# Performance work log

Measured on AMD Instinct MI355X. Metric: run time of the kernel, lower is better.

The kernel has to match this reference:

```python
import jax, jax.numpy as jnp
import numpy as np

D = 256        # d_model
DL = 256       # d_latent
S = 2048       # seq_len
B = 8          # batches
F = 8192       # facts per batch (padded)
MAXPOS = 4096
MAXPRED = 1024
NROLE = 64 + 2 # role_emb rows


def setup_inputs() -> dict:
    key = jax.random.key(0)
    ks = jax.random.split(key, 16)
    def nrm(k, shape, s=0.02):
        return jax.random.normal(k, shape, jnp.float32) * s
    return {
        "pos_emb": nrm(ks[0], (MAXPOS, D)),
        "pred_emb": nrm(ks[1], (MAXPRED, D)),
        "role_emb": nrm(ks[2], (NROLE, D)),
        "w1": nrm(ks[3], (3 * D, 2 * D)), "b1": jnp.zeros((2 * D,), jnp.float32),
        "w2": nrm(ks[4], (2 * D, D)),     "b2": jnp.zeros((D,), jnp.float32),
        "ln_g": jnp.ones((D,), jnp.float32), "ln_b": jnp.zeros((D,), jnp.float32),
        "lw1": nrm(ks[5], (D, DL)), "lb1": jnp.zeros((DL,), jnp.float32),
        "lw2": nrm(ks[6], (DL, DL)), "lb2": jnp.zeros((DL,), jnp.float32),
        "pred_idx": jax.random.randint(ks[7], (B, F), 0, MAXPRED),
        "a0": jax.random.randint(ks[8], (B, F), 0, S),
        "a1": jax.random.randint(ks[9], (B, F), 0, S),
        "role_idx": jax.random.randint(ks[10], (B, F), 0, NROLE),
        "is_role": jax.random.randint(ks[11], (B, F), 0, 2).astype(jnp.int32),
        "add_rev": jax.random.randint(ks[12], (B, F), 0, 2).astype(jnp.int32),
        "mask": jax.random.randint(ks[13], (B, F), 0, 2).astype(jnp.int32),
        "seq_len": S,
    }


def reference(pos_emb, pred_emb, role_emb, w1, b1, w2, b2, ln_g, ln_b,
              lw1, lb1, lw2, lb2,
              pred_idx, a0, a1, role_idx, is_role, add_rev, mask, seq_len):
    nodes = pos_emb[:seq_len]                 # [S, D] shared across batches
    pe = pred_emb[pred_idx]                   # [B, F, D]
    n0 = nodes[a0]                            # [B, F, D]
    n1 = nodes[a1]                            # [B, F, D]
    re = role_emb[role_idx]                   # [B, F, D]

    role_b = is_role.astype(bool)
    valid = mask.astype(bool)

    third = jnp.where(role_b[..., None], re, n1)
    x_fwd = jnp.concatenate([n0, pe, third], axis=-1)   # [B, F, 3D]
    x_rev = jnp.concatenate([n1, pe, n0], axis=-1)      # [B, F, 3D]

    def mlp(x):
        h = jax.nn.gelu(x @ w1 + b1, approximate=False)
        return h @ w2 + b2

    msg_fwd = mlp(x_fwd)                      # [B, F, D]
    msg_rev = mlp(x_rev)                      # [B, F, D]

    w_fwd = valid[..., None].astype(msg_fwd.dtype)
    w_rev = (valid & (~role_b) & add_rev.astype(bool))[..., None].astype(msg_rev.dtype)
    tgt_fwd = jnp.where(role_b, a0, a1)       # role msgs go to tok=a0, binary to a1

    def scat(msg, idx, w):
        return jax.ops.segment_sum(msg * w, idx, num_segments=seq_len)

    agg = jax.vmap(scat)(msg_fwd, tgt_fwd, w_fwd)
    agg = agg + jax.vmap(scat)(msg_rev, a0, w_rev)      # [B, S, D]

    x = nodes[None, :, :] + agg
    mu = jnp.mean(x, axis=-1, keepdims=True)
    var = jnp.mean(jnp.square(x - mu), axis=-1, keepdims=True)
    x = (x - mu) / jnp.sqrt(var + 1e-5) * ln_g + ln_b   # LayerNorm

    pooled = jnp.mean(x, axis=1)              # [B, D]
    h = jax.nn.gelu(pooled @ lw1 + lb1, approximate=False)
    return h @ lw2 + lb2                      # [B, DL]
```

## Files before the change

kernel.cpp:

```cpp
#include <hip/hip_runtime.h>
#include <hip/hip_bf16.h>
#include <cstdint>

#define S_LEN 2048
#define DIM   256
#define NBAT  8
#define NEDGE 65536
#define HID   512
#define INDIM 768

#define OFF_AGG   0u
#define OFF_POOL  16777216u
#define OFF_CNT   16785408u
#define OFF_NODES 16785664u
#define OFF_PRED  17834240u
#define OFF_ROLE  18358528u
#define OFF_W1P   18392576u
#define OFF_W2P   19179008u
#define OFF_FWD   19441152u
#define OFF_REV   19703296u
#define ZERO_BYTES 16785664u

typedef short bshort8 __attribute__((ext_vector_type(8)));
typedef float floatx4 __attribute__((ext_vector_type(4)));
typedef ushort ushort4v __attribute__((ext_vector_type(4)));

__device__ __forceinline__ float gelu_f(float x) {
  return 0.5f * x * (1.0f + erff(x * 0.70710678118654752f));
}
__device__ __forceinline__ ushort f2bf(float v) {
  __hip_bfloat16 h = __float2bfloat16(v);
  return *reinterpret_cast<ushort*>(&h);
}

#define Z4 1049104
#define T4 200832
#define WN 524288
__global__ void prep_all(const float* __restrict__ pos, const float* __restrict__ pred,
                         const float* __restrict__ role,
                         const float* __restrict__ w1, const float* __restrict__ w2,
                         unsigned char* __restrict__ ws) {
  int i = blockIdx.x * blockDim.x + threadIdx.x;
  if (i < Z4) {
    reinterpret_cast<float4*>(ws)[i] = float4{0.f, 0.f, 0.f, 0.f};
    return;
  }
  i -= Z4;
  if (i < T4) {
    const int NN4 = 131072, NP4 = 65536;
    float4 v;
    if (i < NN4) v = reinterpret_cast<const float4*>(pos)[i];
    else if (i < NN4 + NP4) v = reinterpret_cast<const float4*>(pred)[i - NN4];
    else v = reinterpret_cast<const float4*>(role)[i - NN4 - NP4];
    ushort4v h;
    h.x = f2bf(v.x); h.y = f2bf(v.y); h.z = f2bf(v.z); h.w = f2bf(v.w);
    *reinterpret_cast<ushort4v*>((ushort*)(ws + OFF_NODES) + (i << 2)) = h;
    return;
  }
  i -= T4;
  if (i < WN) {
    ushort* W1p = (ushort*)(ws + OFF_W1P);
    ushort* W2p = (ushort*)(ws + OFF_W2P);
    const int N1 = INDIM * HID;
    if (i < N1) {
      int k = i >> 9, n = i & 511;
      W1p[(((k >> 3) << 9) + n) * 8 + (k & 7)] = f2bf(w1[i]);
    } else {
      int j = i - N1;
      int k = j >> 8, n = j & 255;
      W2p[(((k >> 3) << 8) + n) * 8 + (k & 7)] = f2bf(w2[j]);
    }
  }
}

__global__ void build_lists(const int* __restrict__ mask, const int* __restrict__ is_role,
                            const int* __restrict__ add_rev,
                            int* __restrict__ fwd, int* __restrict__ rev, int* __restrict__ cnt) {
  int e = blockIdx.x * blockDim.x + threadIdx.x;
  int lane = threadIdx.x & 63;
  bool c0 = mask[e] != 0;
  bool c1 = c0 && !is_role[e] && add_rev[e];
  unsigned long long b0 = __ballot(c0);
  unsigned long long b1m = __ballot(c1);
  unsigned long long lt = (1ull << lane) - 1ull;
  int base0 = 0, base1 = 0;
  if (lane == 0) {
    base0 = atomicAdd(&cnt[0], __popcll(b0));
    base1 = atomicAdd(&cnt[1], __popcll(b1m));
  }
  base0 = __shfl(base0, 0);
  base1 = __shfl(base1, 0);
  if (c0) fwd[base0 + __popcll(b0 & lt)] = e;
  if (c1) rev[base1 + __popcll(b1m & lt)] = e;
}

#define HSTR_E 520
__global__ __launch_bounds__(512, 4)
void mlp_kernel(const int* __restrict__ cnt, const int* __restrict__ fwd, const int* __restrict__ rev,
                const int* __restrict__ a0, const int* __restrict__ a1,
                const int* __restrict__ pred_idx, const int* __restrict__ role_idx,
                const int* __restrict__ is_role,
                const ushort* __restrict__ T,
                const ushort* __restrict__ W1p, const ushort* __restrict__ W2p,
                const float* __restrict__ b1, const float* __restrict__ b2,
                float* __restrict__ agg) {
  __shared__ ushort Hs[64 * HSTR_E];
  __shared__ int ltgt[64];
  __shared__ int lbat[64];
  __shared__ uint loff[64][3];

  const int tid = threadIdx.x;
  const int nf = cnt[0], nr = cnt[1];
  const int total = nf + nr;
  const int row0 = blockIdx.x * 64;
  if (row0 >= total) return;

  if (tid < 64) {
    int grow = row0 + tid;
    int tgt = -1, bb = 0; uint o0 = 0, o1 = 0, o2 = 0;
    if (grow < total) {
      bool rv = grow >= nf;
      int e = rv ? rev[grow - nf] : fwd[grow];
      bb = e >> 13;
      int A0 = a0[e], A1 = a1[e];
      o1 = 524288u + ((uint)pred_idx[e] << 8);
      if (rv)              { o0 = (uint)A1 << 8; o2 = (uint)A0 << 8;                      tgt = A0; }
      else if (is_role[e]) { o0 = (uint)A0 << 8; o2 = 786432u + ((uint)role_idx[e] << 8); tgt = A0; }
      else                 { o0 = (uint)A0 << 8; o2 = (uint)A1 << 8;                      tgt = A1; }
    }
    ltgt[tid] = tgt; lbat[tid] = bb;
    loff[tid][0] = o0; loff[tid][1] = o1; loff[tid][2] = o2;
  }
  __syncthreads();

  const int lane = tid & 63, wave = tid >> 6;
  const int wm = wave >> 2, wn = wave & 3;
  const int l15 = lane & 15, kb = lane >> 4;
  const int m0 = wm * 32 + l15;
  const int m1 = m0 + 16;

  const uint o00 = loff[m0][0], o01 = loff[m0][1], o02 = loff[m0][2];
  const uint o10 = loff[m1][0], o11 = loff[m1][1], o12 = loff[m1][2];

  floatx4 acc1[2][8];
#pragma unroll
  for (int fm = 0; fm < 2; ++fm)
#pragma unroll
    for (int fn = 0; fn < 8; ++fn) acc1[fm][fn] = (floatx4){0.f, 0.f, 0.f, 0.f};

  const int kcb = kb * 8;
  bshort8 xb0 = *reinterpret_cast<const bshort8*>(T + o00 + kcb);
  bshort8 xb1 = *reinterpret_cast<const bshort8*>(T + o10 + kcb);
#pragma unroll 1
  for (int k0 = 0; k0 < INDIM; k0 += 32) {
    int k1 = k0 + 32;
    uint po0 = (k1 < 256) ? o00 : (k1 < 512) ? o01 : o02;
    uint po1 = (k1 < 256) ? o10 : (k1 < 512) ? o11 : o12;
    int kc1 = (k1 & 255) + kcb;
    bshort8 nx0 = *reinterpret_cast<const bshort8*>(T + po0 + kc1);
    bshort8 nx1 = *reinterpret_cast<const bshort8*>(T + po1 + kc1);

    const ushort* wp = W1p + ((((k0 >> 3) + kb) << 9) + wn * 128 + l15) * 8;
#pragma unroll
    for (int fn = 0; fn < 8; ++fn) {
      bshort8 wv = *reinterpret_cast<const bshort8*>(wp + (fn << 7));
      acc1[0][fn] = __builtin_amdgcn_mfma_f32_16x16x32_bf16(wv, xb0, acc1[0][fn], 0, 0, 0);
      acc1[1][fn] = __builtin_amdgcn_mfma_f32_16x16x32_bf16(wv, xb1, acc1[1][fn], 0, 0, 0);
    }
    xb0 = nx0; xb1 = nx1;
  }

#pragma unroll
  for (int fm = 0; fm < 2; ++fm) {
    int m = fm ? m1 : m0;
#pragma unroll
    for (int fn = 0; fn < 8; ++fn) {
      int n0 = wn * 128 + fn * 16 + kb * 4;
      float4 bb4 = *reinterpret_cast<const float4*>(b1 + n0);
      ushort4v hv;
      hv.x = f2bf(gelu_f(acc1[fm][fn][0] + bb4.x));
      hv.y = f2bf(gelu_f(acc1[fm][fn][1] + bb4.y));
      hv.z = f2bf(gelu_f(acc1[fm][fn][2] + bb4.z));
      hv.w = f2bf(gelu_f(acc1[fm][fn][3] + bb4.w));
      *reinterpret_cast<ushort4v*>(Hs + m * HSTR_E + n0) = hv;
    }
  }
  __syncthreads();

  floatx4 acc2[2][4];
#pragma unroll
  for (int fm = 0; fm < 2; ++fm)
#pragma unroll
    for (int fn = 0; fn < 4; ++fn) acc2[fm][fn] = (floatx4){0.f, 0.f, 0.f, 0.f};

#pragma unroll 1
  for (int k0 = 0; k0 < HID; k0 += 32) {
    bshort8 ha0 = *reinterpret_cast<const bshort8*>(Hs + m0 * HSTR_E + k0 + kcb);
    bshort8 ha1 = *reinterpret_cast<const bshort8*>(Hs + m1 * HSTR_E + k0 + kcb);
    const ushort* wp2 = W2p + ((((k0 >> 3) + kb) << 8) + wn * 64 + l15) * 8;
#pragma unroll
    for (int fn = 0; fn < 4; ++fn) {
      bshort8 wv = *reinterpret_cast<const bshort8*>(wp2 + (fn << 7));
      acc2[0][fn] = __builtin_amdgcn_mfma_f32_16x16x32_bf16(ha0, wv, acc2[0][fn], 0, 0, 0);
      acc2[1][fn] = __builtin_amdgcn_mfma_f32_16x16x32_bf16(ha1, wv, acc2[1][fn], 0, 0, 0);
    }
  }

#pragma unroll
  for (int fn = 0; fn < 4; ++fn) {
    int n = wn * 64 + fn * 16 + l15;
    float bias = b2[n];
#pragma unroll
    for (int fm = 0; fm < 2; ++fm) {
#pragma unroll
      for (int rg = 0; rg < 4; ++rg) {
        int m = wm * 32 + fm * 16 + kb * 4 + rg;
        int tgt = ltgt[m];
        if (tgt >= 0) {
          unsafeAtomicAdd(agg + ((((uint)lbat[m] << 11) + (uint)tgt) << 8) + n,
                          acc2[fm][fn][rg] + bias);
        }
      }
    }
  }
}

__global__ void ln_pool(const float* __restrict__ pos, const float* __restrict__ agg,
                        const float* __restrict__ g, const float* __restrict__ be,
                        float* __restrict__ pooled_sum) {
  __shared__ float r2[16];
  const int b = blockIdx.x >> 7;
  const int sb = blockIdx.x & 127;
  const int t = threadIdx.x;
  const float gg = g[t], bb = be[t];
  const int wv = t >> 6;
  float psum = 0.f;
#pragma unroll 1
  for (int i = 0; i < 16; ++i) {
    int s = sb * 16 + i;
    float x = pos[s * DIM + t] + agg[((b << 11) + s) * DIM + t];
    float a = x, q = x * x;
#pragma unroll
    for (int o = 32; o > 0; o >>= 1) { a += __shfl_xor(a, o); q += __shfl_xor(q, o); }
    if ((t & 63) == 0) { r2[wv * 2] = a; r2[wv * 2 + 1] = q; }
    __syncthreads();
    a = r2[0] + r2[2] + r2[4] + r2[6];
    q = r2[1] + r2[3] + r2[5] + r2[7];
    __syncthreads();
    float mu = a * (1.f / 256.f);
    float var = q * (1.f / 256.f) - mu * mu;
    float y = (x - mu) * rsqrtf(var + 1e-5f) * gg + bb;
    psum += y;
  }
  unsafeAtomicAdd(&pooled_sum[(b << 8) + t], psum);
}

__global__ void final_mlp(const float* __restrict__ pooled_sum,
                          const float* __restrict__ lw1, const float* __restrict__ lb1,
                          const float* __restrict__ lw2, const float* __restrict__ lb2,
                          float* __restrict__ out) {
  __shared__ float pl[256];
  __shared__ float hl[256];
  const int r = blockIdx.x, t = threadIdx.x;
  pl[t] = pooled_sum[(r << 8) + t] * (1.f / 2048.f);
  __syncthreads();
  float a = lb1[t];
#pragma unroll 8
  for (int d = 0; d < 256; ++d) a = fmaf(pl[d], lw1[(d << 8) + t], a);
  hl[t] = gelu_f(a);
  __syncthreads();
  float o = lb2[t];
#pragma unroll 8
  for (int d = 0; d < 256; ++d) o = fmaf(hl[d], lw2[(d << 8) + t], o);
  out[(r << 8) + t] = o;
}

extern "C" void kernel_launch(void* const* d_in, const int* in_sizes, int n_in,
                              void* d_out, int out_size, void* d_ws, size_t ws_size,
                              hipStream_t stream) {
  const float* pos_emb  = (const float*)d_in[0];
  const float* pred_emb = (const float*)d_in[1];
  const float* role_emb = (const float*)d_in[2];
  const float* w1   = (const float*)d_in[3];
  const float* b1   = (const float*)d_in[4];
  const float* w2   = (const float*)d_in[5];
  const float* b2   = (const float*)d_in[6];
  const float* ln_g = (const float*)d_in[7];
  const float* ln_b = (const float*)d_in[8];
  const float* lw1  = (const float*)d_in[9];
  const float* lb1  = (const float*)d_in[10];
  const float* lw2  = (const float*)d_in[11];
  const float* lb2  = (const float*)d_in[12];
  const int* pred_idx = (const int*)d_in[13];
  const int* a0       = (const int*)d_in[14];
  const int* a1       = (const int*)d_in[15];
  const int* role_idx = (const int*)d_in[16];
  const int* is_role  = (const int*)d_in[17];
  const int* add_rev  = (const int*)d_in[18];
  const int* mask     = (const int*)d_in[19];

  unsigned char* ws = (unsigned char*)d_ws;
  float*  agg    = (float*)(ws + OFF_AGG);
  float*  pooled = (float*)(ws + OFF_POOL);
  int*    cnt    = (int*)(ws + OFF_CNT);
  ushort* T      = (ushort*)(ws + OFF_NODES);
  ushort* W1p    = (ushort*)(ws + OFF_W1P);
  ushort* W2p    = (ushort*)(ws + OFF_W2P);
  int*    fwd    = (int*)(ws + OFF_FWD);
  int*    rev    = (int*)(ws + OFF_REV);

  prep_all<<<6931, 256, 0, stream>>>(pos_emb, pred_emb, role_emb, w1, w2, ws);
  build_lists<<<256, 256, 0, stream>>>(mask, is_role, add_rev, fwd, rev, cnt);
  mlp_kernel<<<2048, 512, 0, stream>>>(cnt, fwd, rev, a0, a1, pred_idx, role_idx, is_role,
                                       T, W1p, W2p, b1, b2, agg);
  ln_pool<<<1024, 256, 0, stream>>>(pos_emb, agg, ln_g, ln_b, pooled);
  final_mlp<<<8, 256, 0, stream>>>(pooled, lw1, lb1, lw2, lb2, (float*)d_out);
}
```

Before: 289.9 us.

## Double MLP row tile to 128 per block and aggregate atomics per block in list build

The MLP kernel now processes 128 edge rows per block instead of 64, with each wave holding four 16-row fragments. Each weight fragment loaded from global memory is therefore reused across twice as many MFMAs, halving weight traffic per row. The cost is a larger register footprint, with launch bounds relaxed to 2 blocks per SM, and roughly double the LDS per block. build_lists now combines per-wave counts in shared memory so only one atomic per block hits the global counters.

```diff
diff --git a/kernel.cpp b/kernel.cpp
--- a/kernel.cpp
+++ b/kernel.cpp
@@ -76,26 +76,32 @@
 __global__ void build_lists(const int* __restrict__ mask, const int* __restrict__ is_role,
                             const int* __restrict__ add_rev,
                             int* __restrict__ fwd, int* __restrict__ rev, int* __restrict__ cnt) {
-  int e = blockIdx.x * blockDim.x + threadIdx.x;
-  int lane = threadIdx.x & 63;
+  __shared__ int wc0[4], wc1[4], base[2];
+  int tid = threadIdx.x;
+  int e = blockIdx.x * 256 + tid;
+  int lane = tid & 63, w = tid >> 6;
   bool c0 = mask[e] != 0;
   bool c1 = c0 && !is_role[e] && add_rev[e];
   unsigned long long b0 = __ballot(c0);
   unsigned long long b1m = __ballot(c1);
   unsigned long long lt = (1ull << lane) - 1ull;
-  int base0 = 0, base1 = 0;
-  if (lane == 0) {
-    base0 = atomicAdd(&cnt[0], __popcll(b0));
-    base1 = atomicAdd(&cnt[1], __popcll(b1m));
-  }
-  base0 = __shfl(base0, 0);
-  base1 = __shfl(base1, 0);
-  if (c0) fwd[base0 + __popcll(b0 & lt)] = e;
-  if (c1) rev[base1 + __popcll(b1m & lt)] = e;
+  if (lane == 0) { wc0[w] = __popcll(b0); wc1[w] = __popcll(b1m); }
+  __syncthreads();
+  if (tid == 0) {
+    base[0] = atomicAdd(&cnt[0], wc0[0] + wc0[1] + wc0[2] + wc0[3]);
+    base[1] = atomicAdd(&cnt[1], wc1[0] + wc1[1] + wc1[2] + wc1[3]);
+  }
+  __syncthreads();
+  int p0 = base[0], p1 = base[1];
+  for (int ww = 0; ww < 4; ++ww) {
+    if (ww < w) { p0 += wc0[ww]; p1 += wc1[ww]; }
+  }
+  if (c0) fwd[p0 + __popcll(b0 & lt)] = e;
+  if (c1) rev[p1 + __popcll(b1m & lt)] = e;
 }
 
 #define HSTR_E 520
-__global__ __launch_bounds__(512, 4)
+__global__ __launch_bounds__(512, 2)
 void mlp_kernel(const int* __restrict__ cnt, const int* __restrict__ fwd, const int* __restrict__ rev,
                 const int* __restrict__ a0, const int* __restrict__ a1,
                 const int* __restrict__ pred_idx, const int* __restrict__ role_idx,
@@ -104,18 +110,18 @@
                 const ushort* __restrict__ W1p, const ushort* __restrict__ W2p,
                 const float* __restrict__ b1, const float* __restrict__ b2,
                 float* __restrict__ agg) {
-  __shared__ ushort Hs[64 * HSTR_E];
-  __shared__ int ltgt[64];
-  __shared__ int lbat[64];
-  __shared__ uint loff[64][3];
+  __shared__ ushort Hs[128 * HSTR_E];
+  __shared__ int ltgt[128];
+  __shared__ int lbat[128];
+  __shared__ uint loff[128][3];
 
   const int tid = threadIdx.x;
   const int nf = cnt[0], nr = cnt[1];
   const int total = nf + nr;
-  const int row0 = blockIdx.x * 64;
+  const int row0 = blockIdx.x * 128;
   if (row0 >= total) return;
 
-  if (tid < 64) {
+  if (tid < 128) {
     int grow = row0 + tid;
     int tgt = -1, bb = 0; uint o0 = 0, o1 = 0, o2 = 0;
     if (grow < total) {
@@ -136,73 +142,84 @@
   const int lane = tid & 63, wave = tid >> 6;
   const int wm = wave >> 2, wn = wave & 3;
   const int l15 = lane & 15, kb = lane >> 4;
-  const int m0 = wm * 32 + l15;
-  const int m1 = m0 + 16;
-
-  const uint o00 = loff[m0][0], o01 = loff[m0][1], o02 = loff[m0][2];
-  const uint o10 = loff[m1][0], o11 = loff[m1][1], o12 = loff[m1][2];
-
-  floatx4 acc1[2][8];
-#pragma unroll
-  for (int fm = 0; fm < 2; ++fm)
-#pragma unroll
-    for (int fn = 0; fn < 8; ++fn) acc1[fm][fn] = (floatx4){0.f, 0.f, 0.f, 0.f};
-
   const int kcb = kb * 8;
-  bshort8 xb0 = *reinterpret_cast<const bshort8*>(T + o00 + kcb);
-  bshort8 xb1 = *reinterpret_cast<const bshort8*>(T + o10 + kcb);
+
+  uint off[4][3];
+#pragma unroll
+  for (int fr = 0; fr < 4; ++fr) {
+    int m = wm * 64 + fr * 16 + l15;
+    off[fr][0] = loff[m][0]; off[fr][1] = loff[m][1]; off[fr][2] = loff[m][2];
+  }
+
+  floatx4 acc1[4][8];
+#pragma unroll
+  for (int fr = 0; fr < 4; ++fr)
+#pragma unroll
+    for (int fn = 0; fn < 8; ++fn) acc1[fr][fn] = (floatx4){0.f, 0.f, 0.f, 0.f};
+
+  bshort8 xb[4];
+#pragma unroll
+  for (int fr = 0; fr < 4; ++fr)
+    xb[fr] = *reinterpret_cast<const bshort8*>(T + off[fr][0] + kcb);
+
 #pragma unroll 1
   for (int k0 = 0; k0 < INDIM; k0 += 32) {
     int k1 = k0 + 32;
-    uint po0 = (k1 < 256) ? o00 : (k1 < 512) ? o01 : o02;
-    uint po1 = (k1 < 256) ? o10 : (k1 < 512) ? o11 : o12;
     int kc1 = (k1 & 255) + kcb;
-    bshort8 nx0 = *reinterpret_cast<const bshort8*>(T + po0 + kc1);
-    bshort8 nx1 = *reinterpret_cast<const bshort8*>(T + po1 + kc1);
-
+    bshort8 nx[4];
+#pragma unroll
+    for (int fr = 0; fr < 4; ++fr) {
+      uint po = (k1 < 256) ? off[fr][0] : (k1 < 512) ? off[fr][1] : off[fr][2];
+      nx[fr] = *reinterpret_cast<const bshort8*>(T + po + kc1);
+    }
     const ushort* wp = W1p + ((((k0 >> 3) + kb) << 9) + wn * 128 + l15) * 8;
 #pragma unroll
     for (int fn = 0; fn < 8; ++fn) {
       bshort8 wv = *reinterpret_cast<const bshort8*>(wp + (fn << 7));
-      acc1[0][fn] = __builtin_amdgcn_mfma_f32_16x16x32_bf16(wv, xb0, acc1[0][fn], 0, 0, 0);
-      acc1[1][fn] = __builtin_amdgcn_mfma_f32_16x16x32_bf16(wv, xb1, acc1[1][fn], 0, 0, 0);
-    }
-    xb0 = nx0; xb1 = nx1;
-  }
-
-#pragma unroll
-  for (int fm = 0; fm < 2; ++fm) {
-    int m = fm ? m1 : m0;
+#pragma unroll
+      for (int fr = 0; fr < 4; ++fr)
+        acc1[fr][fn] = __builtin_amdgcn_mfma_f32_16x16x32_bf16(wv, xb[fr], acc1[fr][fn], 0, 0, 0);
+    }
+#pragma unroll
+    for (int fr = 0; fr < 4; ++fr) xb[fr] = nx[fr];
+  }
+
+#pragma unroll
+  for (int fr = 0; fr < 4; ++fr) {
+    int m = wm * 64 + fr * 16 + l15;
 #pragma unroll
     for (int fn = 0; fn < 8; ++fn) {
       int n0 = wn * 128 + fn * 16 + kb * 4;
       float4 bb4 = *reinterpret_cast<const float4*>(b1 + n0);
       ushort4v hv;
-      hv.x = f2bf(gelu_f(acc1[fm][fn][0] + bb4.x));
-      hv.y = f2bf(gelu_f(acc1[fm][fn][1] + bb4.y));
-      hv.z = f2bf(gelu_f(acc1[fm][fn][2] + bb4.z));
-      hv.w = f2bf(gelu_f(acc1[fm][fn][3] + bb4.w));
+      hv.x = f2bf(gelu_f(acc1[fr][fn][0] + bb4.x));
+      hv.y = f2bf(gelu_f(acc1[fr][fn][1] + bb4.y));
+      hv.z = f2bf(gelu_f(acc1[fr][fn][2] + bb4.z));
+      hv.w = f2bf(gelu_f(acc1[fr][fn][3] + bb4.w));
       *reinterpret_cast<ushort4v*>(Hs + m * HSTR_E + n0) = hv;
     }
   }
   __syncthreads();
 
-  floatx4 acc2[2][4];
-#pragma unroll
-  for (int fm = 0; fm < 2; ++fm)
-#pragma unroll
-    for (int fn = 0; fn < 4; ++fn) acc2[fm][fn] = (floatx4){0.f, 0.f, 0.f, 0.f};
+  floatx4 acc2[4][4];
+#pragma unroll
+  for (int fr = 0; fr < 4; ++fr)
+#pragma unroll
+    for (int fn = 0; fn < 4; ++fn) acc2[fr][fn] = (floatx4){0.f, 0.f, 0.f, 0.f};
 
 #pragma unroll 1
   for (int k0 = 0; k0 < HID; k0 += 32) {
-    bshort8 ha0 = *reinterpret_cast<const bshort8*>(Hs + m0 * HSTR_E + k0 + kcb);
-    bshort8 ha1 = *reinterpret_cast<const bshort8*>(Hs + m1 * HSTR_E + k0 + kcb);
+    bshort8 ha[4];
+#pragma unroll
+    for (int fr = 0; fr < 4; ++fr)
+      ha[fr] = *reinterpret_cast<const bshort8*>(Hs + (wm * 64 + fr * 16 + l15) * HSTR_E + k0 + kcb);
     const ushort* wp2 = W2p + ((((k0 >> 3) + kb) << 8) + wn * 64 + l15) * 8;
 #pragma unroll
     for (int fn = 0; fn < 4; ++fn) {
       bshort8 wv = *reinterpret_cast<const bshort8*>(wp2 + (fn << 7));
-      acc2[0][fn] = __builtin_amdgcn_mfma_f32_16x16x32_bf16(ha0, wv, acc2[0][fn], 0, 0, 0);
-      acc2[1][fn] = __builtin_amdgcn_mfma_f32_16x16x32_bf16(ha1, wv, acc2[1][fn], 0, 0, 0);
+#pragma unroll
+      for (int fr = 0; fr < 4; ++fr)
+        acc2[fr][fn] = __builtin_amdgcn_mfma_f32_16x16x32_bf16(ha[fr], wv, acc2[fr][fn], 0, 0, 0);
     }
   }
 
@@ -211,14 +228,14 @@
     int n = wn * 64 + fn * 16 + l15;
     float bias = b2[n];
 #pragma unroll
-    for (int fm = 0; fm < 2; ++fm) {
+    for (int fr = 0; fr < 4; ++fr) {
 #pragma unroll
       for (int rg = 0; rg < 4; ++rg) {
-        int m = wm * 32 + fm * 16 + kb * 4 + rg;
+        int m = wm * 64 + fr * 16 + kb * 4 + rg;
         int tgt = ltgt[m];
         if (tgt >= 0) {
           unsafeAtomicAdd(agg + ((((uint)lbat[m] << 11) + (uint)tgt) << 8) + n,
-                          acc2[fm][fn][rg] + bias);
+                          acc2[fr][fn][rg] + bias);
         }
       }
     }
@@ -311,7 +328,7 @@
 
   prep_all<<<6931, 256, 0, stream>>>(pos_emb, pred_emb, role_emb, w1, w2, ws);
   build_lists<<<256, 256, 0, stream>>>(mask, is_role, add_rev, fwd, rev, cnt);
-  mlp_kernel<<<2048, 512, 0, stream>>>(cnt, fwd, rev, a0, a1, pred_idx, role_idx, is_role,
+  mlp_kernel<<<1024, 512, 0, stream>>>(cnt, fwd, rev, a0, a1, pred_idx, role_idx, is_role,
                                        T, W1p, W2p, b1, b2, agg);
   ln_pool<<<1024, 256, 0, stream>>>(pos_emb, agg, ln_g, ln_b, pooled);
   final_mlp<<<8, 256, 0, stream>>>(pooled, lw1, lb1, lw2, lb2, (float*)d_out);
```

Result: slower. 308.6 us (+6.5%).
